# Performance work log

Measured on AMD Instinct MI355X. Metric: run time of the kernel, lower is better.

## Reference

```python
import jax, jax.numpy as jnp
import numpy as np

N = 50000      # nodes
E = 400000     # edges (avg degree 8)
G = 64         # graphs in batch
IN_DIM = 128
OUT_DIM = 16


def _linear_params(key, fan_in, fan_out):
    k1, k2 = jax.random.split(key)
    s = 1.0 / np.sqrt(fan_in)
    W = jax.random.uniform(k1, (fan_in, fan_out), minval=-s, maxval=s, dtype=jnp.float32)
    b = jax.random.uniform(k2, (fan_out,), minval=-s, maxval=s, dtype=jnp.float32)
    return W, b


def setup_inputs() -> dict:
    key = jax.random.key(0)
    ks = jax.random.split(key, 12)
    x = jax.random.normal(ks[0], (N, IN_DIM), dtype=jnp.float32)
    edge_index = jax.random.randint(ks[1], (2, E), 0, N)
    # balanced graph assignment (sorted, every graph id present)
    batch = (jnp.arange(N) * G) // N
    W1, b1 = _linear_params(ks[2], IN_DIM, 64)
    W2, b2 = _linear_params(ks[3], 64, 256)
    W3, b3 = _linear_params(ks[4], 256, 512)
    W4, b4 = _linear_params(ks[5], 512, 64)
    Wr, br = _linear_params(ks[6], IN_DIM, 64)
    fc1_W, fc1_b = _linear_params(ks[7], 64, 64)
    fc2_W, fc2_b = _linear_params(ks[8], 64, OUT_DIM)
    ln_g = jnp.ones((64,), jnp.float32); ln_b = jnp.zeros((64,), jnp.float32)
    fcn_g = jnp.ones((64,), jnp.float32); fcn_b = jnp.zeros((64,), jnp.float32)
    return dict(x=x, edge_index=edge_index, batch=batch,
                W1=W1, b1=b1, W2=W2, b2=b2, W3=W3, b3=b3, W4=W4, b4=b4,
                Wr=Wr, br=br, ln_g=ln_g, ln_b=ln_b,
                fc1_W=fc1_W, fc1_b=fc1_b, fcn_g=fcn_g, fcn_b=fcn_b,
                fc2_W=fc2_W, fc2_b=fc2_b)


def _leaky_relu(h):
    return jnp.where(h >= 0, h, 0.01 * h)


def _layer_norm(h, g, b, eps=1e-5):
    m = jnp.mean(h, axis=-1, keepdims=True)
    v = jnp.var(h, axis=-1, keepdims=True)
    return (h - m) * jax.lax.rsqrt(v + eps) * g + b


def reference(x, edge_index, batch, W1, b1, W2, b2, W3, b3, W4, b4,
              Wr, br, ln_g, ln_b, fc1_W, fc1_b, fcn_g, fcn_b, fc2_W, fc2_b):
    src, dst = edge_index[0], edge_index[1]
    n = x.shape[0]
    # PyG GCNConv normalization with self-loops: deg = 1 + in-degree
    deg = jax.ops.segment_sum(jnp.ones(src.shape[0], x.dtype), dst, num_segments=n) + 1.0
    dis = jax.lax.rsqrt(deg)                 # [N]
    edge_norm = (dis[src] * dis[dst])[:, None]   # [E,1]
    self_norm = (dis * dis)[:, None]             # [N,1]

    def gcn_conv(h, W, b):
        h = h @ W                                            # transform first (PyG order)
        agg = jax.ops.segment_sum(h[src] * edge_norm, dst, num_segments=n)
        return agg + h * self_norm + b                       # self-loop term + bias

    residual = x @ Wr + br
    h = _leaky_relu(gcn_conv(x, W1, b1))
    h = _leaky_relu(gcn_conv(h, W2, b2))
    h = _leaky_relu(gcn_conv(h, W3, b3))
    h = _leaky_relu(gcn_conv(h, W4, b4))
    h = _layer_norm(h + residual, ln_g, ln_b)
    # global max pool over graphs
    p = jax.ops.segment_max(h, batch, num_segments=G)        # [G,64]
    p = _layer_norm(p @ fc1_W + fc1_b, fcn_g, fcn_b)
    p = _leaky_relu(p)
    return p @ fc2_W + fc2_b                                 # [G,16]
```

## Files before the change

### kernel.cpp

```cpp
#include <hip/hip_runtime.h>
#include <hip/hip_bf16.h>
#include <math.h>

typedef short bf16x8 __attribute__((ext_vector_type(8)));
typedef short bf16x4 __attribute__((ext_vector_type(4)));
typedef float f32x4 __attribute__((ext_vector_type(4)));

__device__ inline unsigned short f2bf(float f) {
  unsigned u = __float_as_uint(f);
  u += 0x7FFF + ((u >> 16) & 1);
  return (unsigned short)(u >> 16);
}
__device__ inline float bf2f(unsigned short h) {
  return __uint_as_float(((unsigned)h) << 16);
}
__device__ inline float bflo(unsigned u) { return __uint_as_float(u << 16); }
__device__ inline float bfhi(unsigned u) { return __uint_as_float(u & 0xffff0000u); }


__global__ __launch_bounds__(256) void count_k(const int* __restrict__ dst, int* __restrict__ cnt, int e) {
  int i = blockIdx.x * 256 + threadIdx.x;
  if (i < e) atomicAdd(&cnt[dst[i]], 1);
}

__global__ __launch_bounds__(256) void scan_a(const int* __restrict__ cnt, int* __restrict__ bsum, int n) {
  int i = blockIdx.x * 256 + threadIdx.x;
  int v = (i < n) ? cnt[i] : 0;
#pragma unroll
  for (int o = 32; o > 0; o >>= 1) v += __shfl_xor(v, o);
  __shared__ int ws[4];
  if ((threadIdx.x & 63) == 0) ws[threadIdx.x >> 6] = v;
  __syncthreads();
  if (threadIdx.x == 0) bsum[blockIdx.x] = ws[0] + ws[1] + ws[2] + ws[3];
}

__global__ __launch_bounds__(256) void scan_b(const int* __restrict__ bsum, int* __restrict__ bpre,
                                              int* __restrict__ off_n, int nb) {
  __shared__ int s[256];
  int t = threadIdx.x;
  int v = (t < nb) ? bsum[t] : 0;
  s[t] = v;
  __syncthreads();
  for (int o = 1; o < 256; o <<= 1) {
    int u = (t >= o) ? s[t - o] : 0;
    __syncthreads();
    s[t] += u;
    __syncthreads();
  }
  if (t < nb) bpre[t] = s[t] - v;
  if (t == 255) off_n[0] = s[255];
}

__global__ __launch_bounds__(256) void scan_c(const int* __restrict__ cnt, const int* __restrict__ bpre,
                                              int* __restrict__ off, int* __restrict__ cursor,
                                              float* __restrict__ dis, int n) {
  __shared__ int s[256];
  int i = blockIdx.x * 256 + threadIdx.x;
  int t = threadIdx.x;
  int v = (i < n) ? cnt[i] : 0;
  s[t] = v;
  __syncthreads();
  for (int o = 1; o < 256; o <<= 1) {
    int u = (t >= o) ? s[t - o] : 0;
    __syncthreads();
    s[t] += u;
    __syncthreads();
  }
  if (i < n) {
    int ov = bpre[blockIdx.x] + s[t] - v;
    off[i] = ov;
    cursor[i] = ov;
    dis[i] = rsqrtf((float)v + 1.0f);
  }
}

__global__ __launch_bounds__(256) void scatter_k(const int* __restrict__ src, const int* __restrict__ dst,
                                                 int* __restrict__ cursor, int* __restrict__ csr, int e) {
  int i = blockIdx.x * 256 + threadIdx.x;
  if (i < e) {
    int p = atomicAdd(&cursor[dst[i]], 1);
    csr[p] = src[i];
  }
}


__global__ __launch_bounds__(256) void wconv_k(const float* __restrict__ W1, const float* __restrict__ Wr,
                                               const float* __restrict__ W2, const float* __restrict__ W3,
                                               const float* __restrict__ W4,
                                               short* __restrict__ o1, short* __restrict__ oR,
                                               short* __restrict__ o2, short* __restrict__ o3,
                                               short* __restrict__ o4) {
  int b = blockIdx.x;
  const float* W; short* O; int K, N, nr;
  if (b < 64)       { W = W1; O = o1; K = 128; N = 64;  nr = b; }
  else if (b < 128) { W = Wr; O = oR; K = 128; N = 64;  nr = b - 64; }
  else if (b < 384) { W = W2; O = o2; K = 64;  N = 256; nr = b - 128; }
  else if (b < 896) { W = W3; O = o3; K = 256; N = 512; nr = b - 384; }
  else              { W = W4; O = o4; K = 512; N = 64;  nr = b - 896; }
  for (int k = threadIdx.x; k < K; k += 256)
    O[(size_t)nr * K + k] = (short)f2bf(W[(size_t)k * N + nr]);
}


template<int KT, int NTOT, int WM, int WN, int BIAS, int RELU, int ABF, int OBF, int SPLIT, int SCL, int BLK>
__global__ __launch_bounds__(256, BLK) void mgemm(const void* __restrict__ Av,
                                                  const short* __restrict__ Wc,
                                                  const float* __restrict__ bias,
                                                  void* __restrict__ Cv, void* __restrict__ Cv2,
                                                  const float* __restrict__ scl, int M) {
  __shared__ short As[64 * WM][ABF ? 40 : 72];
  __shared__ short Bs[64 * WN][40];
  const int tid = threadIdx.x;
  const int row0 = blockIdx.x * (64 * WM);
  const int col0 = blockIdx.y * (64 * WN);
  const int w = tid >> 6, lane = tid & 63;
  const int wm = w / WN, wn = w % WN;
  const int rm = wm * 64, cn = wn * 64;
  const int lm = lane & 15, lk = (lane >> 4) * 8;

  f32x4 acc[4][4];
#pragma unroll
  for (int i = 0; i < 4; i++)
#pragma unroll
    for (int j = 0; j < 4; j++)
#pragma unroll
      for (int r = 0; r < 4; r++) acc[i][j][r] = 0.f;

  for (int k0 = 0; k0 < KT; k0 += 32) {
#pragma unroll
    for (int p = 0; p < WM; p++) {
      int r = (tid >> 2) + p * 64;
      int kseg = (tid & 3) * 8;
      int gr = row0 + r;
      if (ABF) {
        bf16x8 v = {0, 0, 0, 0, 0, 0, 0, 0};
        if (gr < M) v = *(const bf16x8*)((const short*)Av + (size_t)gr * KT + k0 + kseg);
        *(bf16x8*)&As[r][kseg] = v;
      } else {
        float4 v0 = {0.f, 0.f, 0.f, 0.f}, v1 = {0.f, 0.f, 0.f, 0.f};
        if (gr < M) {
          const float* ap = (const float*)Av + (size_t)gr * KT + k0 + kseg;
          v0 = *(const float4*)ap;
          v1 = *(const float4*)(ap + 4);
        }
        float vv[8] = {v0.x, v0.y, v0.z, v0.w, v1.x, v1.y, v1.z, v1.w};
        bf16x8 hv, lv;
#pragma unroll
        for (int j = 0; j < 8; j++) {
          unsigned short h = f2bf(vv[j]);
          hv[j] = (short)h;
          lv[j] = (short)f2bf(vv[j] - bf2f(h));
        }
        *(bf16x8*)&As[r][kseg] = hv;
        *(bf16x8*)&As[r][32 + kseg] = lv;
      }
    }
#pragma unroll
    for (int p = 0; p < WN; p++) {
      int nr = (tid >> 2) + p * 64;
      int seg = (tid & 3) * 8;
      *(bf16x8*)&Bs[nr][seg] = *(const bf16x8*)(Wc + (size_t)(col0 + nr) * KT + k0 + seg);
    }
    __syncthreads();

    bf16x8 ah[4], al[4], bb[4];
#pragma unroll
    for (int mt = 0; mt < 4; mt++) {
      ah[mt] = *(const bf16x8*)&As[rm + mt * 16 + lm][lk];
      if (!ABF) al[mt] = *(const bf16x8*)&As[rm + mt * 16 + lm][32 + lk];
    }
#pragma unroll
    for (int nt = 0; nt < 4; nt++) bb[nt] = *(const bf16x8*)&Bs[cn + nt * 16 + lm][lk];
#pragma unroll
    for (int mt = 0; mt < 4; mt++)
#pragma unroll
      for (int nt = 0; nt < 4; nt++) {
        acc[mt][nt] = __builtin_amdgcn_mfma_f32_16x16x32_bf16(ah[mt], bb[nt], acc[mt][nt], 0, 0, 0);
        if (!ABF)
          acc[mt][nt] = __builtin_amdgcn_mfma_f32_16x16x32_bf16(al[mt], bb[nt], acc[mt][nt], 0, 0, 0);
      }
    __syncthreads();
  }

  if (SPLIT) {
    short* epi = (short*)&As[0][0];
    if (wn == 0) {
#pragma unroll
      for (int mt = 0; mt < 4; mt++) {
        int lr = rm + mt * 16 + (lane >> 4) * 4;
#pragma unroll
        for (int r = 0; r < 4; r++) {
          int gr = row0 + lr + r;
          float sc = (SCL && gr < M) ? scl[gr] : 0.f;
#pragma unroll
          for (int nt = 0; nt < 4; nt++)
            epi[(lr + r) * 64 + nt * 16 + lm] = (short)f2bf(acc[mt][nt][r] * sc);
        }
      }
    } else {
#pragma unroll
      for (int mt = 0; mt < 4; mt++) {
        int grb = row0 + rm + mt * 16 + (lane >> 4) * 4;
#pragma unroll
        for (int nt = 0; nt < 4; nt++) {
          int gc = nt * 16 + lm;
          float bv = bias[gc];
#pragma unroll
          for (int r = 0; r < 4; r++) {
            int gr = grb + r;
            if (gr < M) ((float*)Cv2)[(size_t)gr * 64 + gc] = acc[mt][nt][r] + bv;
          }
        }
      }
    }
    __syncthreads();
    int base = tid * 32;
    int row = base >> 6, col = base & 63;
    int gr = row0 + row;
    if (gr < M) {
#pragma unroll
      for (int q = 0; q < 4; q++)
        *(bf16x8*)((short*)Cv + (size_t)gr * 64 + col + q * 8) = *(bf16x8*)&epi[base + q * 8];
    }
  } else if (OBF && WM == 1) {
    short* epi = &Bs[0][0];
    const int NCOL = 64 * WN;
    float bvv[4];
#pragma unroll
    for (int nt = 0; nt < 4; nt++) bvv[nt] = BIAS ? bias[col0 + cn + nt * 16 + lm] : 0.f;
#pragma unroll
    for (int mt = 0; mt < 4; mt++) {
      __syncthreads();
#pragma unroll
      for (int r = 0; r < 4; r++) {
        int gr = row0 + mt * 16 + (lane >> 4) * 4 + r;
        float sc = (SCL && gr < M) ? scl[gr] : 1.f;
#pragma unroll
        for (int nt = 0; nt < 4; nt++) {
          float v = acc[mt][nt][r] + bvv[nt];
          if (RELU) v = (v >= 0.f) ? v : 0.01f * v;
          if (SCL) v *= sc;
          epi[((lane >> 4) * 4 + r) * NCOL + cn + nt * 16 + lm] = (short)f2bf(v);
        }
      }
      __syncthreads();
      const int per = (16 * NCOL) / 256;
      int base = tid * per;
      int lr = base / NCOL, lc = base % NCOL;
      int gr = row0 + mt * 16 + lr;
      if (gr < M) {
#pragma unroll
        for (int q = 0; q < per / 8; q++)
          *(bf16x8*)((short*)Cv + (size_t)gr * NTOT + col0 + lc + q * 8) = *(bf16x8*)&epi[base + q * 8];
      }
    }
  } else {
#pragma unroll
    for (int mt = 0; mt < 4; mt++) {
      int grb = row0 + rm + mt * 16 + (lane >> 4) * 4;
#pragma unroll
      for (int nt = 0; nt < 4; nt++) {
        int gc = col0 + cn + nt * 16 + lm;
        float bv = BIAS ? bias[gc] : 0.f;
#pragma unroll
        for (int r = 0; r < 4; r++) {
          int gr = grb + r;
          if (gr < M) {
            float v = acc[mt][nt][r] + bv;
            if (RELU) v = (v >= 0.f) ? v : 0.01f * v;
            if (SCL) v *= scl[gr];
            if (OBF) ((short*)Cv)[(size_t)gr * NTOT + gc] = (short)f2bf(v);
            else     ((float*)Cv)[(size_t)gr * NTOT + gc] = v;
          }
        }
      }
    }
  }
}


__global__ __launch_bounds__(256, 3) void fused34_k(const short* __restrict__ z3,
                                                    const short* __restrict__ W3c,
                                                    const float* __restrict__ b3,
                                                    const short* __restrict__ W4c,
                                                    const float* __restrict__ dis,
                                                    short* __restrict__ T4, int M) {
  __shared__ short Bs[2][32][264];
  __shared__ short Ws4[2][64][40];
  __shared__ short Hs[64][40];
  const int tid = threadIdx.x;
  const int row0 = blockIdx.x * 64;
  const int w = tid >> 6, lane = tid & 63;
  const int lm = lane & 15, lk = (lane >> 4) * 8;
  const int rquad = (lane >> 4) * 4;
  const int w4row = tid >> 2, w4seg = (tid & 3) * 8;

  bf16x8 afr[8];
  {
    int gr = row0 + w * 16 + lm;
    bool ok = gr < M;
    const short* zp = z3 + (size_t)gr * 256 + lk;
#pragma unroll
    for (int kc = 0; kc < 8; kc++) {
      bf16x8 v = {0, 0, 0, 0, 0, 0, 0, 0};
      if (ok) v = *(const bf16x8*)(zp + kc * 32);
      afr[kc] = v;
    }
  }

  f32x4 t4acc[4];
#pragma unroll
  for (int nt = 0; nt < 4; nt++)
#pragma unroll
    for (int r = 0; r < 4; r++) t4acc[nt][r] = 0.f;

  bf16x8 pw3[4];
  bf16x8 pw4;
#pragma unroll
  for (int q = 0; q < 4; q++) {
    int flat = q * 2048 + tid * 8;
    pw3[q] = *(const bf16x8*)(W3c + flat);
  }
  pw4 = *(const bf16x8*)(W4c + (size_t)w4row * 512 + w4seg);
#pragma unroll
  for (int q = 0; q < 4; q++) {
    int flat = q * 2048 + tid * 8;
    *(bf16x8*)&Bs[0][flat >> 8][flat & 255] = pw3[q];
  }
  *(bf16x8*)&Ws4[0][w4row][w4seg] = pw4;
  __syncthreads();

  for (int c = 0; c < 16; c++) {
    int cur = c & 1, nxt = cur ^ 1;
    if (c < 15) {
#pragma unroll
      for (int q = 0; q < 4; q++) {
        int flat = q * 2048 + tid * 8;
        pw3[q] = *(const bf16x8*)(W3c + (size_t)(c + 1) * 32 * 256 + flat);
      }
      pw4 = *(const bf16x8*)(W4c + (size_t)w4row * 512 + (c + 1) * 32 + w4seg);
    }

    f32x4 acc1[2];
#pragma unroll
    for (int nt = 0; nt < 2; nt++)
#pragma unroll
      for (int r = 0; r < 4; r++) acc1[nt][r] = 0.f;
#pragma unroll
    for (int k0 = 0; k0 < 8; k0++) {
      bf16x8 bb[2];
#pragma unroll
      for (int nt = 0; nt < 2; nt++) bb[nt] = *(const bf16x8*)&Bs[cur][nt * 16 + lm][k0 * 32 + lk];
#pragma unroll
      for (int nt = 0; nt < 2; nt++)
        acc1[nt] = __builtin_amdgcn_mfma_f32_16x16x32_bf16(afr[k0], bb[nt], acc1[nt], 0, 0, 0);
    }
#pragma unroll
    for (int nt = 0; nt < 2; nt++) {
      float bv = b3[c * 32 + nt * 16 + lm];
#pragma unroll
      for (int r = 0; r < 4; r++) {
        float v = acc1[nt][r] + bv;
        v = (v >= 0.f) ? v : 0.01f * v;
        Hs[w * 16 + rquad + r][nt * 16 + lm] = (short)f2bf(v);
      }
    }
    {
      bf16x8 ah2 = *(const bf16x8*)&Hs[w * 16 + lm][lk];
      bf16x8 bb2[4];
#pragma unroll
      for (int nt = 0; nt < 4; nt++) bb2[nt] = *(const bf16x8*)&Ws4[cur][nt * 16 + lm][lk];
#pragma unroll
      for (int nt = 0; nt < 4; nt++)
        t4acc[nt] = __builtin_amdgcn_mfma_f32_16x16x32_bf16(ah2, bb2[nt], t4acc[nt], 0, 0, 0);
    }
    if (c < 15) {
#pragma unroll
      for (int q = 0; q < 4; q++) {
        int flat = q * 2048 + tid * 8;
        *(bf16x8*)&Bs[nxt][flat >> 8][flat & 255] = pw3[q];
      }
      *(bf16x8*)&Ws4[nxt][w4row][w4seg] = pw4;
    }
    __syncthreads();
  }
  short* epi = (short*)&Bs[0][0][0];
#pragma unroll
  for (int r = 0; r < 4; r++) {
    int lr = w * 16 + rquad + r;
    int gr = row0 + lr;
    float sc = (gr < M) ? dis[gr] : 0.f;
#pragma unroll
    for (int nt = 0; nt < 4; nt++)
      epi[lr * 64 + nt * 16 + lm] = (short)f2bf(t4acc[nt][r] * sc);
  }
  __syncthreads();
  {
    int base = tid * 16;
    int row = base >> 6, col = base & 63;
    int gr = row0 + row;
    if (gr < M) {
      *(bf16x8*)(T4 + (size_t)gr * 64 + col)     = *(bf16x8*)&epi[base];
      *(bf16x8*)(T4 + (size_t)gr * 64 + col + 8) = *(bf16x8*)&epi[base + 8];
    }
  }
}


template<int BR, int OSCL>
__global__ __launch_bounds__(256) void aggb64_k(const short* __restrict__ T, const float* __restrict__ dis,
                                                const int* __restrict__ off, const int* __restrict__ csr,
                                                const float* __restrict__ bias, short* __restrict__ Out, int n) {
  int wv = (blockIdx.x * 256 + threadIdx.x) >> 6;
  int lane = threadIdx.x & 63;
  int qtr = lane >> 4, ql = lane & 15;
  int wid = wv * 4 + qtr;
  if (wid >= n) return;
  float di = dis[wid];
  int e0 = off[wid], e1 = off[wid + 1];
  const uint2* Tw = (const uint2*)T;
  uint2 su = Tw[(size_t)wid * 16 + ql];
  float a0 = bflo(su.x), a1 = bfhi(su.x), a2 = bflo(su.y), a3 = bfhi(su.y);
  int e = e0;
  for (; e + 8 <= e1; e += 8) {
    uint2 u0 = Tw[(size_t)csr[e]     * 16 + ql];
    uint2 u1 = Tw[(size_t)csr[e + 1] * 16 + ql];
    uint2 u2 = Tw[(size_t)csr[e + 2] * 16 + ql];
    uint2 u3 = Tw[(size_t)csr[e + 3] * 16 + ql];
    uint2 u4 = Tw[(size_t)csr[e + 4] * 16 + ql];
    uint2 u5 = Tw[(size_t)csr[e + 5] * 16 + ql];
    uint2 u6 = Tw[(size_t)csr[e + 6] * 16 + ql];
    uint2 u7 = Tw[(size_t)csr[e + 7] * 16 + ql];
    a0 += ((bflo(u0.x) + bflo(u1.x)) + (bflo(u2.x) + bflo(u3.x))) +
          ((bflo(u4.x) + bflo(u5.x)) + (bflo(u6.x) + bflo(u7.x)));
    a1 += ((bfhi(u0.x) + bfhi(u1.x)) + (bfhi(u2.x) + bfhi(u3.x))) +
          ((bfhi(u4.x) + bfhi(u5.x)) + (bfhi(u6.x) + bfhi(u7.x)));
    a2 += ((bflo(u0.y) + bflo(u1.y)) + (bflo(u2.y) + bflo(u3.y))) +
          ((bflo(u4.y) + bflo(u5.y)) + (bflo(u6.y) + bflo(u7.y)));
    a3 += ((bfhi(u0.y) + bfhi(u1.y)) + (bfhi(u2.y) + bfhi(u3.y))) +
          ((bfhi(u4.y) + bfhi(u5.y)) + (bfhi(u6.y) + bfhi(u7.y)));
  }
  for (; e + 4 <= e1; e += 4) {
    uint2 u0 = Tw[(size_t)csr[e]     * 16 + ql];
    uint2 u1 = Tw[(size_t)csr[e + 1] * 16 + ql];
    uint2 u2 = Tw[(size_t)csr[e + 2] * 16 + ql];
    uint2 u3 = Tw[(size_t)csr[e + 3] * 16 + ql];
    a0 += (bflo(u0.x) + bflo(u1.x)) + (bflo(u2.x) + bflo(u3.x));
    a1 += (bfhi(u0.x) + bfhi(u1.x)) + (bfhi(u2.x) + bfhi(u3.x));
    a2 += (bflo(u0.y) + bflo(u1.y)) + (bflo(u2.y) + bflo(u3.y));
    a3 += (bfhi(u0.y) + bfhi(u1.y)) + (bfhi(u2.y) + bfhi(u3.y));
  }
  for (; e < e1; e++) {
    uint2 u = Tw[(size_t)csr[e] * 16 + ql];
    a0 += bflo(u.x); a1 += bfhi(u.x); a2 += bflo(u.y); a3 += bfhi(u.y);
  }
  float v0 = di * a0, v1 = di * a1, v2 = di * a2, v3 = di * a3;
  if (BR) {
    v0 += bias[ql * 4];     v1 += bias[ql * 4 + 1];
    v2 += bias[ql * 4 + 2]; v3 += bias[ql * 4 + 3];
    v0 = (v0 >= 0.f) ? v0 : 0.01f * v0;
    v1 = (v1 >= 0.f) ? v1 : 0.01f * v1;
    v2 = (v2 >= 0.f) ? v2 : 0.01f * v2;
    v3 = (v3 >= 0.f) ? v3 : 0.01f * v3;
  }
  if (OSCL) { v0 *= di; v1 *= di; v2 *= di; v3 *= di; }
  uint2 o;
  o.x = (unsigned)f2bf(v0) | ((unsigned)f2bf(v1) << 16);
  o.y = (unsigned)f2bf(v2) | ((unsigned)f2bf(v3) << 16);
  ((uint2*)Out)[(size_t)wid * 16 + ql] = o;
}

__global__ __launch_bounds__(256) void agg64_ln_k(const short* __restrict__ T, const float* __restrict__ dis,
                                                  const int* __restrict__ off, const int* __restrict__ csr,
                                                  const float* __restrict__ bias, const float* __restrict__ resid,
                                                  const float* __restrict__ g, const float* __restrict__ b,
                                                  float* __restrict__ outh, int n) {
  int wv = (blockIdx.x * 256 + threadIdx.x) >> 6;
  int lane = threadIdx.x & 63;
  int qtr = lane >> 4, ql = lane & 15;
  int wid = wv * 4 + qtr;
  if (wid >= n) return;
  float di = dis[wid];
  int e0 = off[wid], e1 = off[wid + 1];
  const uint2* Tw = (const uint2*)T;
  uint2 su = Tw[(size_t)wid * 16 + ql];
  float a0 = bflo(su.x), a1 = bfhi(su.x), a2 = bflo(su.y), a3 = bfhi(su.y);
  int e = e0;
  for (; e + 8 <= e1; e += 8) {
    uint2 u0 = Tw[(size_t)csr[e]     * 16 + ql];
    uint2 u1 = Tw[(size_t)csr[e + 1] * 16 + ql];
    uint2 u2 = Tw[(size_t)csr[e + 2] * 16 + ql];
    uint2 u3 = Tw[(size_t)csr[e + 3] * 16 + ql];
    uint2 u4 = Tw[(size_t)csr[e + 4] * 16 + ql];
    uint2 u5 = Tw[(size_t)csr[e + 5] * 16 + ql];
    uint2 u6 = Tw[(size_t)csr[e + 6] * 16 + ql];
    uint2 u7 = Tw[(size_t)csr[e + 7] * 16 + ql];
    a0 += ((bflo(u0.x) + bflo(u1.x)) + (bflo(u2.x) + bflo(u3.x))) +
          ((bflo(u4.x) + bflo(u5.x)) + (bflo(u6.x) + bflo(u7.x)));
    a1 += ((bfhi(u0.x) + bfhi(u1.x)) + (bfhi(u2.x) + bfhi(u3.x))) +
          ((bfhi(u4.x) + bfhi(u5.x)) + (bfhi(u6.x) + bfhi(u7.x)));
    a2 += ((bflo(u0.y) + bflo(u1.y)) + (bflo(u2.y) + bflo(u3.y))) +
          ((bflo(u4.y) + bflo(u5.y)) + (bflo(u6.y) + bflo(u7.y)));
    a3 += ((bfhi(u0.y) + bfhi(u1.y)) + (bfhi(u2.y) + bfhi(u3.y))) +
          ((bfhi(u4.y) + bfhi(u5.y)) + (bfhi(u6.y) + bfhi(u7.y)));
  }
  for (; e + 4 <= e1; e += 4) {
    uint2 u0 = Tw[(size_t)csr[e]     * 16 + ql];
    uint2 u1 = Tw[(size_t)csr[e + 1] * 16 + ql];
    uint2 u2 = Tw[(size_t)csr[e + 2] * 16 + ql];
    uint2 u3 = Tw[(size_t)csr[e + 3] * 16 + ql];
    a0 += (bflo(u0.x) + bflo(u1.x)) + (bflo(u2.x) + bflo(u3.x));
    a1 += (bfhi(u0.x) + bfhi(u1.x)) + (bfhi(u2.x) + bfhi(u3.x));
    a2 += (bflo(u0.y) + bflo(u1.y)) + (bflo(u2.y) + bflo(u3.y));
    a3 += (bfhi(u0.y) + bfhi(u1.y)) + (bfhi(u2.y) + bfhi(u3.y));
  }
  for (; e < e1; e++) {
    uint2 u = Tw[(size_t)csr[e] * 16 + ql];
    a0 += bflo(u.x); a1 += bfhi(u.x); a2 += bflo(u.y); a3 += bfhi(u.y);
  }
  float4 rv = ((const float4*)resid)[(size_t)wid * 16 + ql];
  float v0 = di * a0 + bias[ql * 4];
  float v1 = di * a1 + bias[ql * 4 + 1];
  float v2 = di * a2 + bias[ql * 4 + 2];
  float v3 = di * a3 + bias[ql * 4 + 3];
  v0 = (v0 >= 0.f) ? v0 : 0.01f * v0;
  v1 = (v1 >= 0.f) ? v1 : 0.01f * v1;
  v2 = (v2 >= 0.f) ? v2 : 0.01f * v2;
  v3 = (v3 >= 0.f) ? v3 : 0.01f * v3;
  v0 += rv.x; v1 += rv.y; v2 += rv.z; v3 += rv.w;
  float s = (v0 + v1) + (v2 + v3);
  float ss = (v0 * v0 + v1 * v1) + (v2 * v2 + v3 * v3);
#pragma unroll
  for (int o = 8; o > 0; o >>= 1) {
    s += __shfl_xor(s, o);
    ss += __shfl_xor(ss, o);
  }
  float m = s * (1.f / 64.f);
  float var = ss * (1.f / 64.f) - m * m;
  float rs = rsqrtf(var + 1e-5f);
  float4 o4;
  o4.x = (v0 - m) * rs * g[ql * 4]     + b[ql * 4];
  o4.y = (v1 - m) * rs * g[ql * 4 + 1] + b[ql * 4 + 1];
  o4.z = (v2 - m) * rs * g[ql * 4 + 2] + b[ql * 4 + 2];
  o4.w = (v3 - m) * rs * g[ql * 4 + 3] + b[ql * 4 + 3];
  ((float4*)outh)[(size_t)wid * 16 + ql] = o4;
}

__global__ __launch_bounds__(256) void agg256b_k(const short* __restrict__ T, const float* __restrict__ dis,
                                                 const int* __restrict__ off, const int* __restrict__ csr,
                                                 short* __restrict__ Out, int n) {
  int wv = (blockIdx.x * 256 + threadIdx.x) >> 6;
  int lane = threadIdx.x & 63;
  int qtr = lane >> 4, ql = lane & 15;
  int wid = wv * 4 + qtr;
  if (wid >= n) return;
  float di = dis[wid];
  int e0 = off[wid], e1 = off[wid + 1];
  const short* base = T + (size_t)wid * 256 + ql * 16;
  bf16x8 s0 = *(const bf16x8*)base;
  bf16x8 s1 = *(const bf16x8*)(base + 8);
  float a[16];
#pragma unroll
  for (int q = 0; q < 8; q++) { a[q] = bf2f((unsigned short)s0[q]); a[8 + q] = bf2f((unsigned short)s1[q]); }
  int e = e0;
  for (; e + 4 <= e1; e += 4) {
    const short* p0 = T + (size_t)csr[e]     * 256 + ql * 16;
    const short* p1 = T + (size_t)csr[e + 1] * 256 + ql * 16;
    const short* p2 = T + (size_t)csr[e + 2] * 256 + ql * 16;
    const short* p3 = T + (size_t)csr[e + 3] * 256 + ql * 16;
    bf16x8 t00 = *(const bf16x8*)p0, t01 = *(const bf16x8*)(p0 + 8);
    bf16x8 t10 = *(const bf16x8*)p1, t11 = *(const bf16x8*)(p1 + 8);
    bf16x8 t20 = *(const bf16x8*)p2, t21 = *(const bf16x8*)(p2 + 8);
    bf16x8 t30 = *(const bf16x8*)p3, t31 = *(const bf16x8*)(p3 + 8);
#pragma unroll
    for (int q = 0; q < 8; q++) {
      a[q] += (bf2f((unsigned short)t00[q]) + bf2f((unsigned short)t10[q])) +
              (bf2f((unsigned short)t20[q]) + bf2f((unsigned short)t30[q]));
      a[8 + q] += (bf2f((unsigned short)t01[q]) + bf2f((unsigned short)t11[q])) +
                  (bf2f((unsigned short)t21[q]) + bf2f((unsigned short)t31[q]));
    }
  }
  for (; e < e1; e++) {
    const short* p = T + (size_t)csr[e] * 256 + ql * 16;
    bf16x8 t0 = *(const bf16x8*)p, t1 = *(const bf16x8*)(p + 8);
#pragma unroll
    for (int q = 0; q < 8; q++) {
      a[q] += bf2f((unsigned short)t0[q]);
      a[8 + q] += bf2f((unsigned short)t1[q]);
    }
  }
  bf16x8 o0, o1;
#pragma unroll
  for (int q = 0; q < 8; q++) {
    o0[q] = (short)f2bf(di * a[q]);
    o1[q] = (short)f2bf(di * a[8 + q]);
  }
  short* ob = Out + (size_t)wid * 256 + ql * 16;
  *(bf16x8*)ob = o0;
  *(bf16x8*)(ob + 8) = o1;
}


__global__ __launch_bounds__(256) void pool_mlp_k(const float* __restrict__ hn,
                                                  const float* __restrict__ fc1W, const float* __restrict__ fc1b,
                                                  const float* __restrict__ fng, const float* __restrict__ fnb,
                                                  const float* __restrict__ fc2W, const float* __restrict__ fc2b,
                                                  float* __restrict__ out, int n) {
  const int G = 64;
  int g = blockIdx.x;
  int f = threadIdx.x & 63, c = threadIdx.x >> 6;
  long long s0 = ((long long)g * n + G - 1) / G;
  long long e0 = ((long long)(g + 1) * n + G - 1) / G;
  float m = -INFINITY;
  for (long long i = s0 + c; i < e0; i += 4) m = fmaxf(m, hn[(size_t)i * 64 + f]);
  __shared__ float red[4][64];
  __shared__ float ps[64], qs[64];
  red[c][f] = m;
  __syncthreads();
  if (c == 0) ps[f] = fmaxf(fmaxf(red[0][f], red[1][f]), fmaxf(red[2][f], red[3][f]));
  __syncthreads();
  if (threadIdx.x < 64) {
    int lane = threadIdx.x;
    float q = fc1b[lane];
#pragma unroll 8
    for (int k = 0; k < 64; k++) q = fmaf(ps[k], fc1W[k * 64 + lane], q);
    float s = q, ss = q * q;
#pragma unroll
    for (int o = 32; o > 0; o >>= 1) {
      s += __shfl_xor(s, o);
      ss += __shfl_xor(ss, o);
    }
    float mm = s * (1.f / 64.f);
    float var = ss * (1.f / 64.f) - mm * mm;
    float y = (q - mm) * rsqrtf(var + 1e-5f) * fng[lane] + fnb[lane];
    y = (y >= 0.f) ? y : 0.01f * y;
    qs[lane] = y;
    __builtin_amdgcn_wave_barrier();
    if (lane < 16) {
      float o = fc2b[lane];
#pragma unroll 8
      for (int k = 0; k < 64; k++) o = fmaf(qs[k], fc2W[k * 16 + lane], o);
      out[g * 16 + lane] = o;
    }
  }
}


extern "C" void kernel_launch(void* const* d_in, const int* in_sizes, int n_in,
                              void* d_out, int out_size, void* d_ws, size_t ws_size,
                              hipStream_t stream) {
  const float* x   = (const float*)d_in[0];
  const int*   ei  = (const int*)d_in[1];
  const float* W1  = (const float*)d_in[3];
  const float* b1  = (const float*)d_in[4];
  const float* W2  = (const float*)d_in[5];
  const float* b2  = (const float*)d_in[6];
  const float* W3  = (const float*)d_in[7];
  const float* b3  = (const float*)d_in[8];
  const float* W4  = (const float*)d_in[9];
  const float* b4  = (const float*)d_in[10];
  const float* Wr  = (const float*)d_in[11];
  const float* br  = (const float*)d_in[12];
  const float* lng = (const float*)d_in[13];
  const float* lnb = (const float*)d_in[14];
  const float* f1W = (const float*)d_in[15];
  const float* f1b = (const float*)d_in[16];
  const float* fng = (const float*)d_in[17];
  const float* fnb = (const float*)d_in[18];
  const float* f2W = (const float*)d_in[19];
  const float* f2b = (const float*)d_in[20];

  int n = in_sizes[0] / 128;
  int e = in_sizes[1] / 2;
  const int* src = ei;
  const int* dst = ei + e;

  float* arena = (float*)d_ws;
  float* resid = arena;
  short* h2b   = (short*)(arena + (size_t)64 * n);
  short* t4b   = (short*)(arena + (size_t)64 * n);
  short* z3b   = (short*)(arena + (size_t)192 * n);
  float* hn    = arena + (size_t)192 * n;
  short* t1b   = (short*)(arena + (size_t)320 * n);
  short* h1b   = (short*)(arena + (size_t)352 * n);
  short* z2b   = (short*)(arena + (size_t)384 * n);
  float* dis   = arena + (size_t)448 * n;
  int* cnt    = (int*)(dis + n);
  int* off    = cnt + n;
  int* cursor = off + n + 1;
  int* csr    = cursor + n;
  int* bsum   = csr + e;
  int* bpre   = bsum + 256;
  float* pool = (float*)(bpre + 256);
  size_t wq = (((size_t)(pool + 4096)) + 15) & ~(size_t)15;
  short* wc1 = (short*)wq;
  short* wcR = wc1 + 8192;
  short* wc2 = wcR + 8192;
  short* wc3 = wc2 + 16384;
  short* wc4 = wc3 + 131072;
  size_t need = ((char*)(wc4 + 32768) - (char*)d_ws) + 64;
  if (ws_size < need) return;

  int nb_n = (n + 255) / 256;
  int nb_e = (e + 255) / 256;
  int nb_w4 = ((n + 3) / 4 + 3) / 4;
  int g_wide = (n + 63) / 64;
  int g_fused = (n + 127) / 128;

  wconv_k<<<960, 256, 0, stream>>>(W1, Wr, W2, W3, W4, wc1, wcR, wc2, wc3, wc4);

  hipMemsetAsync(cnt, 0, (size_t)n * sizeof(int), stream);
  count_k<<<nb_e, 256, 0, stream>>>(dst, cnt, e);
  scan_a<<<nb_n, 256, 0, stream>>>(cnt, bsum, n);
  scan_b<<<1, 256, 0, stream>>>(bsum, bpre, off + n, nb_n);
  scan_c<<<nb_n, 256, 0, stream>>>(cnt, bpre, off, cursor, dis, n);
  scatter_k<<<nb_e, 256, 0, stream>>>(src, dst, cursor, csr, e);

  mgemm<128, 128, 2, 2, 1, 0, 0, 0, 1, 1, 4><<<dim3(g_fused, 1), 256, 0, stream>>>(x, wc1, br, t1b, resid, dis, n);
  aggb64_k<1, 1><<<nb_w4, 256, 0, stream>>>(t1b, dis, off, csr, b1, h1b, n);
  aggb64_k<0, 0><<<nb_w4, 256, 0, stream>>>(h1b, dis, off, csr, nullptr, z2b, n);
  mgemm<64, 256, 1, 4, 1, 1, 1, 1, 0, 1, 5><<<dim3(g_wide, 1), 256, 0, stream>>>(z2b, wc2, b2, h2b, nullptr, dis, n);
  agg256b_k<<<nb_w4, 256, 0, stream>>>(h2b, dis, off, csr, z3b, n);
  fused34_k<<<g_wide, 256, 0, stream>>>(z3b, wc3, b3, wc4, dis, t4b, n);
  agg64_ln_k<<<nb_w4, 256, 0, stream>>>(t4b, dis, off, csr, b4, resid, lng, lnb, hn, n);
  pool_mlp_k<<<64, 256, 0, stream>>>(hn, f1W, f1b, fng, fnb, f2W, f2b, (float*)d_out, n);
}
```

Baseline: 353.6 us.

## Restructure fused layer-3/4 GEMM with 2x2 warp tiling and direct-to-LDS weight loads

Reworks the fused W3→leaky→W4 kernel so each wave computes 32 rows by 16 columns of the W3 chunk, reusing each B fragment across two M tiles. W3 tiles are now streamed with global_load_lds straight into LDS in the MFMA fragment layout, instead of staging through registers. Each wave accumulates layer-4 partial sums over two chunks, reading W4 fragments directly from global memory. The two column-half partials are then reduced through an fp32 LDS buffer in the epilogue. This aims to cut LDS traffic and register staging, at the cost of more accumulator registers, uncached global reads of W4, and an extra fp32 reduction pass.

New measurement: 366.6 us. 3.7% more time.

```diff
diff --git a/kernel.cpp b/kernel.cpp
--- a/kernel.cpp
+++ b/kernel.cpp
@@ -16,6 +16,11 @@
 }
 __device__ inline float bflo(unsigned u) { return __uint_as_float(u << 16); }
 __device__ inline float bfhi(unsigned u) { return __uint_as_float(u & 0xffff0000u); }
+
+__device__ __forceinline__ void gl_lds16(const void* g, void* l) {
+  __builtin_amdgcn_global_load_lds((const __attribute__((address_space(1))) void*)g,
+                                   (__attribute__((address_space(3))) void*)l, 16, 0, 0);
+}
 
 
 __global__ __launch_bounds__(256) void count_k(const int* __restrict__ dst, int* __restrict__ cnt, int e) {
@@ -285,123 +290,128 @@
                                                     const short* __restrict__ W4c,
                                                     const float* __restrict__ dis,
                                                     short* __restrict__ T4, int M) {
-  __shared__ short Bs[2][32][264];
-  __shared__ short Ws4[2][64][40];
-  __shared__ short Hs[64][40];
+  __shared__ __align__(16) char smem[43008];
+  short* Bs = (short*)smem;
   const int tid = threadIdx.x;
   const int row0 = blockIdx.x * 64;
   const int w = tid >> 6, lane = tid & 63;
-  const int lm = lane & 15, lk = (lane >> 4) * 8;
-  const int rquad = (lane >> 4) * 4;
-  const int w4row = tid >> 2, w4seg = (tid & 3) * 8;
-
-  bf16x8 afr[8];
-  {
-    int gr = row0 + w * 16 + lm;
+  const int wr = w >> 1, wc = w & 1;
+  const int q = lane >> 4, lm = lane & 15;
+  short* slab = (short*)(smem + 32768) + w * 1280;
+
+  bf16x8 afr[2][8];
+#pragma unroll
+  for (int mt = 0; mt < 2; mt++) {
+    int gr = row0 + wr * 32 + mt * 16 + lm;
     bool ok = gr < M;
-    const short* zp = z3 + (size_t)gr * 256 + lk;
-#pragma unroll
-    for (int kc = 0; kc < 8; kc++) {
+    const short* zp = z3 + (size_t)gr * 256 + q * 8;
+#pragma unroll
+    for (int k0 = 0; k0 < 8; k0++) {
       bf16x8 v = {0, 0, 0, 0, 0, 0, 0, 0};
-      if (ok) v = *(const bf16x8*)(zp + kc * 32);
-      afr[kc] = v;
-    }
-  }
-
-  f32x4 t4acc[4];
-#pragma unroll
-  for (int nt = 0; nt < 4; nt++)
-#pragma unroll
-    for (int r = 0; r < 4; r++) t4acc[nt][r] = 0.f;
-
-  bf16x8 pw3[4];
-  bf16x8 pw4;
-#pragma unroll
-  for (int q = 0; q < 4; q++) {
-    int flat = q * 2048 + tid * 8;
-    pw3[q] = *(const bf16x8*)(W3c + flat);
-  }
-  pw4 = *(const bf16x8*)(W4c + (size_t)w4row * 512 + w4seg);
-#pragma unroll
-  for (int q = 0; q < 4; q++) {
-    int flat = q * 2048 + tid * 8;
-    *(bf16x8*)&Bs[0][flat >> 8][flat & 255] = pw3[q];
-  }
-  *(bf16x8*)&Ws4[0][w4row][w4seg] = pw4;
+      if (ok) v = *(const bf16x8*)(zp + k0 * 32);
+      afr[mt][k0] = v;
+    }
+  }
+
+  f32x4 t4acc[2][4];
+#pragma unroll
+  for (int mt = 0; mt < 2; mt++)
+#pragma unroll
+    for (int nt = 0; nt < 4; nt++)
+#pragma unroll
+      for (int r = 0; r < 4; r++) t4acc[mt][nt][r] = 0.f;
+
+#pragma unroll
+  for (int i = 0; i < 4; i++) {
+    int seg = w * 4 + i;
+    int k0s = seg >> 1, colT = seg & 1;
+    const short* gsrc = W3c + (size_t)(colT * 16 + lm) * 256 + k0s * 32 + q * 8;
+    gl_lds16(gsrc, Bs + seg * 512);
+  }
   __syncthreads();
 
+#pragma unroll
   for (int c = 0; c < 16; c++) {
-    int cur = c & 1, nxt = cur ^ 1;
+    const int cur = c & 1, nxt = cur ^ 1;
     if (c < 15) {
 #pragma unroll
-      for (int q = 0; q < 4; q++) {
-        int flat = q * 2048 + tid * 8;
-        pw3[q] = *(const bf16x8*)(W3c + (size_t)(c + 1) * 32 * 256 + flat);
-      }
-      pw4 = *(const bf16x8*)(W4c + (size_t)w4row * 512 + (c + 1) * 32 + w4seg);
-    }
+      for (int i = 0; i < 4; i++) {
+        int seg = w * 4 + i;
+        int k0s = seg >> 1, colT = seg & 1;
+        const short* gsrc = W3c + (size_t)((c + 1) * 32 + colT * 16 + lm) * 256 + k0s * 32 + q * 8;
+        gl_lds16(gsrc, Bs + nxt * 8192 + seg * 512);
+      }
+    }
+    float bv = b3[c * 32 + wc * 16 + lm];
 
     f32x4 acc1[2];
 #pragma unroll
-    for (int nt = 0; nt < 2; nt++)
-#pragma unroll
-      for (int r = 0; r < 4; r++) acc1[nt][r] = 0.f;
+    for (int mt = 0; mt < 2; mt++)
+#pragma unroll
+      for (int r = 0; r < 4; r++) acc1[mt][r] = 0.f;
 #pragma unroll
     for (int k0 = 0; k0 < 8; k0++) {
-      bf16x8 bb[2];
-#pragma unroll
-      for (int nt = 0; nt < 2; nt++) bb[nt] = *(const bf16x8*)&Bs[cur][nt * 16 + lm][k0 * 32 + lk];
-#pragma unroll
-      for (int nt = 0; nt < 2; nt++)
-        acc1[nt] = __builtin_amdgcn_mfma_f32_16x16x32_bf16(afr[k0], bb[nt], acc1[nt], 0, 0, 0);
-    }
-#pragma unroll
-    for (int nt = 0; nt < 2; nt++) {
-      float bv = b3[c * 32 + nt * 16 + lm];
+      bf16x8 bb = *(const bf16x8*)(Bs + cur * 8192 + (k0 * 2 + wc) * 512 + lane * 8);
+#pragma unroll
+      for (int mt = 0; mt < 2; mt++)
+        acc1[mt] = __builtin_amdgcn_mfma_f32_16x16x32_bf16(afr[mt][k0], bb, acc1[mt], 0, 0, 0);
+    }
+#pragma unroll
+    for (int mt = 0; mt < 2; mt++)
 #pragma unroll
       for (int r = 0; r < 4; r++) {
-        float v = acc1[nt][r] + bv;
+        float v = acc1[mt][r] + bv;
         v = (v >= 0.f) ? v : 0.01f * v;
-        Hs[w * 16 + rquad + r][nt * 16 + lm] = (short)f2bf(v);
-      }
-    }
-    {
-      bf16x8 ah2 = *(const bf16x8*)&Hs[w * 16 + lm][lk];
-      bf16x8 bb2[4];
-#pragma unroll
-      for (int nt = 0; nt < 4; nt++) bb2[nt] = *(const bf16x8*)&Ws4[cur][nt * 16 + lm][lk];
-#pragma unroll
-      for (int nt = 0; nt < 4; nt++)
-        t4acc[nt] = __builtin_amdgcn_mfma_f32_16x16x32_bf16(ah2, bb2[nt], t4acc[nt], 0, 0, 0);
-    }
-    if (c < 15) {
-#pragma unroll
-      for (int q = 0; q < 4; q++) {
-        int flat = q * 2048 + tid * 8;
-        *(bf16x8*)&Bs[nxt][flat >> 8][flat & 255] = pw3[q];
-      }
-      *(bf16x8*)&Ws4[nxt][w4row][w4seg] = pw4;
+        slab[(mt * 16 + q * 4 + r) * 40 + (c & 1) * 16 + lm] = (short)f2bf(v);
+      }
+    if (c & 1) {
+      bf16x8 ha[2];
+#pragma unroll
+      for (int mt = 0; mt < 2; mt++)
+        ha[mt] = *(const bf16x8*)(slab + (mt * 16 + lm) * 40 + q * 8);
+      int kb = (c - 1 + (q >> 1)) * 32 + wc * 16 + (q & 1) * 8;
+#pragma unroll
+      for (int nt = 0; nt < 4; nt++) {
+        bf16x8 wb = *(const bf16x8*)(W4c + (size_t)(nt * 16 + lm) * 512 + kb);
+#pragma unroll
+        for (int mt = 0; mt < 2; mt++)
+          t4acc[mt][nt] = __builtin_amdgcn_mfma_f32_16x16x32_bf16(ha[mt], wb, t4acc[mt][nt], 0, 0, 0);
+      }
     }
     __syncthreads();
   }
-  short* epi = (short*)&Bs[0][0][0];
-#pragma unroll
-  for (int r = 0; r < 4; r++) {
-    int lr = w * 16 + rquad + r;
-    int gr = row0 + lr;
-    float sc = (gr < M) ? dis[gr] : 0.f;
+
+  float* Pf = (float*)smem;
+#pragma unroll
+  for (int mt = 0; mt < 2; mt++)
 #pragma unroll
     for (int nt = 0; nt < 4; nt++)
-      epi[lr * 64 + nt * 16 + lm] = (short)f2bf(t4acc[nt][r] * sc);
-  }
+#pragma unroll
+      for (int r = 0; r < 4; r++)
+        Pf[wc * 4352 + (size_t)(wr * 32 + mt * 16 + q * 4 + r) * 68 + nt * 16 + lm] = t4acc[mt][nt][r];
   __syncthreads();
   {
-    int base = tid * 16;
-    int row = base >> 6, col = base & 63;
+    int row = tid >> 2, cb = (tid & 3) * 16;
     int gr = row0 + row;
     if (gr < M) {
-      *(bf16x8*)(T4 + (size_t)gr * 64 + col)     = *(bf16x8*)&epi[base];
-      *(bf16x8*)(T4 + (size_t)gr * 64 + col + 8) = *(bf16x8*)&epi[base + 8];
+      float sc = dis[gr];
+      const f32x4* p0 = (const f32x4*)(Pf + (size_t)row * 68 + cb);
+      const f32x4* p1 = (const f32x4*)(Pf + 4352 + (size_t)row * 68 + cb);
+      bf16x8 o0, o1;
+#pragma unroll
+      for (int j2 = 0; j2 < 2; j2++) {
+        f32x4 s = p0[j2] + p1[j2];
+#pragma unroll
+        for (int j = 0; j < 4; j++) o0[j2 * 4 + j] = (short)f2bf(s[j] * sc);
+      }
+#pragma unroll
+      for (int j2 = 0; j2 < 2; j2++) {
+        f32x4 s = p0[2 + j2] + p1[2 + j2];
+#pragma unroll
+        for (int j = 0; j < 4; j++) o1[j2 * 4 + j] = (short)f2bf(s[j] * sc);
+      }
+      *(bf16x8*)(T4 + (size_t)gr * 64 + cb) = o0;
+      *(bf16x8*)(T4 + (size_t)gr * 64 + cb + 8) = o1;
     }
   }
 }
```

## Fuse 256-wide neighbor aggregation into the layer-3/4 fused GEMM kernel

Applied to the files above, without the earlier changes.

The standalone agg256b kernel is removed. fused34_k now gathers neighbor rows of h2 for its own 64-node tile, normalizes them and stages the bf16 result in shared memory (reusing the Bs buffer) before loading the MFMA A fragments. This drops the global write and re-read of the 256-wide z3 intermediate and one kernel launch. In exchange, the gather latency now sits inside a GEMM kernel with limited occupancy (launch bounds 256,3), so it is less hidden, and two extra barriers are added.

After: 352.4 us. Within noise of the previous version (-0.4%).

```diff
diff --git a/kernel.cpp b/kernel.cpp
--- a/kernel.cpp
+++ b/kernel.cpp
@@ -279,7 +279,8 @@
 }
 
 
-__global__ __launch_bounds__(256, 3) void fused34_k(const short* __restrict__ z3,
+__global__ __launch_bounds__(256, 3) void fused34_k(const short* __restrict__ h2,
+                                                    const int* __restrict__ off, const int* __restrict__ csr,
                                                     const short* __restrict__ W3c,
                                                     const float* __restrict__ b3,
                                                     const short* __restrict__ W4c,
@@ -294,19 +295,73 @@
   const int lm = lane & 15, lk = (lane >> 4) * 8;
   const int rquad = (lane >> 4) * 4;
   const int w4row = tid >> 2, w4seg = (tid & 3) * 8;
+  const int qtr = lane >> 4, ql = lane & 15;
+
+  short* Zs = (short*)&Bs[0][0][0];
+  for (int pass = 0; pass < 4; pass++) {
+    int nid = pass * 16 + w * 4 + qtr;
+    int gr = row0 + nid;
+    float a[16];
+    if (gr < M) {
+      float di = dis[gr];
+      int e0 = off[gr], e1 = off[gr + 1];
+      const short* base = h2 + (size_t)gr * 256 + ql * 16;
+      bf16x8 s0 = *(const bf16x8*)base;
+      bf16x8 s1 = *(const bf16x8*)(base + 8);
+#pragma unroll
+      for (int j = 0; j < 8; j++) { a[j] = bf2f((unsigned short)s0[j]); a[8 + j] = bf2f((unsigned short)s1[j]); }
+      int e = e0;
+      for (; e + 4 <= e1; e += 4) {
+        const short* p0 = h2 + (size_t)csr[e]     * 256 + ql * 16;
+        const short* p1 = h2 + (size_t)csr[e + 1] * 256 + ql * 16;
+        const short* p2 = h2 + (size_t)csr[e + 2] * 256 + ql * 16;
+        const short* p3 = h2 + (size_t)csr[e + 3] * 256 + ql * 16;
+        bf16x8 t00 = *(const bf16x8*)p0, t01 = *(const bf16x8*)(p0 + 8);
+        bf16x8 t10 = *(const bf16x8*)p1, t11 = *(const bf16x8*)(p1 + 8);
+        bf16x8 t20 = *(const bf16x8*)p2, t21 = *(const bf16x8*)(p2 + 8);
+        bf16x8 t30 = *(const bf16x8*)p3, t31 = *(const bf16x8*)(p3 + 8);
+#pragma unroll
+        for (int j = 0; j < 8; j++) {
+          a[j] += (bf2f((unsigned short)t00[j]) + bf2f((unsigned short)t10[j])) +
+                  (bf2f((unsigned short)t20[j]) + bf2f((unsigned short)t30[j]));
+          a[8 + j] += (bf2f((unsigned short)t01[j]) + bf2f((unsigned short)t11[j])) +
+                      (bf2f((unsigned short)t21[j]) + bf2f((unsigned short)t31[j]));
+        }
+      }
+      for (; e < e1; e++) {
+        const short* p = h2 + (size_t)csr[e] * 256 + ql * 16;
+        bf16x8 t0 = *(const bf16x8*)p, t1 = *(const bf16x8*)(p + 8);
+#pragma unroll
+        for (int j = 0; j < 8; j++) {
+          a[j] += bf2f((unsigned short)t0[j]);
+          a[8 + j] += bf2f((unsigned short)t1[j]);
+        }
+      }
+#pragma unroll
+      for (int j = 0; j < 16; j++) a[j] *= di;
+    } else {
+#pragma unroll
+      for (int j = 0; j < 16; j++) a[j] = 0.f;
+    }
+    bf16x8 o0, o1;
+#pragma unroll
+    for (int j = 0; j < 8; j++) {
+      o0[j] = (short)f2bf(a[j]);
+      o1[j] = (short)f2bf(a[8 + j]);
+    }
+    *(bf16x8*)&Zs[nid * 264 + ql * 16] = o0;
+    *(bf16x8*)&Zs[nid * 264 + ql * 16 + 8] = o1;
+  }
+  __syncthreads();
 
   bf16x8 afr[8];
   {
-    int gr = row0 + w * 16 + lm;
-    bool ok = gr < M;
-    const short* zp = z3 + (size_t)gr * 256 + lk;
-#pragma unroll
-    for (int kc = 0; kc < 8; kc++) {
-      bf16x8 v = {0, 0, 0, 0, 0, 0, 0, 0};
-      if (ok) v = *(const bf16x8*)(zp + kc * 32);
-      afr[kc] = v;
-    }
-  }
+    int lr = w * 16 + lm;
+#pragma unroll
+    for (int kc = 0; kc < 8; kc++)
+      afr[kc] = *(const bf16x8*)&Zs[lr * 264 + kc * 32 + lk];
+  }
+  __syncthreads();
 
   f32x4 t4acc[4];
 #pragma unroll
@@ -546,60 +601,6 @@
   ((float4*)outh)[(size_t)wid * 16 + ql] = o4;
 }
 
-__global__ __launch_bounds__(256) void agg256b_k(const short* __restrict__ T, const float* __restrict__ dis,
-                                                 const int* __restrict__ off, const int* __restrict__ csr,
-                                                 short* __restrict__ Out, int n) {
-  int wv = (blockIdx.x * 256 + threadIdx.x) >> 6;
-  int lane = threadIdx.x & 63;
-  int qtr = lane >> 4, ql = lane & 15;
-  int wid = wv * 4 + qtr;
-  if (wid >= n) return;
-  float di = dis[wid];
-  int e0 = off[wid], e1 = off[wid + 1];
-  const short* base = T + (size_t)wid * 256 + ql * 16;
-  bf16x8 s0 = *(const bf16x8*)base;
-  bf16x8 s1 = *(const bf16x8*)(base + 8);
-  float a[16];
-#pragma unroll
-  for (int q = 0; q < 8; q++) { a[q] = bf2f((unsigned short)s0[q]); a[8 + q] = bf2f((unsigned short)s1[q]); }
-  int e = e0;
-  for (; e + 4 <= e1; e += 4) {
-    const short* p0 = T + (size_t)csr[e]     * 256 + ql * 16;
-    const short* p1 = T + (size_t)csr[e + 1] * 256 + ql * 16;
-    const short* p2 = T + (size_t)csr[e + 2] * 256 + ql * 16;
-    const short* p3 = T + (size_t)csr[e + 3] * 256 + ql * 16;
-    bf16x8 t00 = *(const bf16x8*)p0, t01 = *(const bf16x8*)(p0 + 8);
-    bf16x8 t10 = *(const bf16x8*)p1, t11 = *(const bf16x8*)(p1 + 8);
-    bf16x8 t20 = *(const bf16x8*)p2, t21 = *(const bf16x8*)(p2 + 8);
-    bf16x8 t30 = *(const bf16x8*)p3, t31 = *(const bf16x8*)(p3 + 8);
-#pragma unroll
-    for (int q = 0; q < 8; q++) {
-      a[q] += (bf2f((unsigned short)t00[q]) + bf2f((unsigned short)t10[q])) +
-              (bf2f((unsigned short)t20[q]) + bf2f((unsigned short)t30[q]));
-      a[8 + q] += (bf2f((unsigned short)t01[q]) + bf2f((unsigned short)t11[q])) +
-                  (bf2f((unsigned short)t21[q]) + bf2f((unsigned short)t31[q]));
-    }
-  }
-  for (; e < e1; e++) {
-    const short* p = T + (size_t)csr[e] * 256 + ql * 16;
-    bf16x8 t0 = *(const bf16x8*)p, t1 = *(const bf16x8*)(p + 8);
-#pragma unroll
-    for (int q = 0; q < 8; q++) {
-      a[q] += bf2f((unsigned short)t0[q]);
-      a[8 + q] += bf2f((unsigned short)t1[q]);
-    }
-  }
-  bf16x8 o0, o1;
-#pragma unroll
-  for (int q = 0; q < 8; q++) {
-    o0[q] = (short)f2bf(di * a[q]);
-    o1[q] = (short)f2bf(di * a[8 + q]);
-  }
-  short* ob = Out + (size_t)wid * 256 + ql * 16;
-  *(bf16x8*)ob = o0;
-  *(bf16x8*)(ob + 8) = o1;
-}
-
 
 __global__ __launch_bounds__(256) void pool_mlp_k(const float* __restrict__ hn,
                                                   const float* __restrict__ fc1W, const float* __restrict__ fc1b,
@@ -678,9 +679,8 @@
   float* arena = (float*)d_ws;
   float* resid = arena;
   short* h2b   = (short*)(arena + (size_t)64 * n);
-  short* t4b   = (short*)(arena + (size_t)64 * n);
-  short* z3b   = (short*)(arena + (size_t)192 * n);
-  float* hn    = arena + (size_t)192 * n;
+  short* t4b   = (short*)(arena + (size_t)192 * n);
+  float* hn    = arena + (size_t)224 * n;
   short* t1b   = (short*)(arena + (size_t)320 * n);
   short* h1b   = (short*)(arena + (size_t)352 * n);
   short* z2b   = (short*)(arena + (size_t)384 * n);
@@ -720,8 +720,7 @@
   aggb64_k<1, 1><<<nb_w4, 256, 0, stream>>>(t1b, dis, off, csr, b1, h1b, n);
   aggb64_k<0, 0><<<nb_w4, 256, 0, stream>>>(h1b, dis, off, csr, nullptr, z2b, n);
   mgemm<64, 256, 1, 4, 1, 1, 1, 1, 0, 1, 5><<<dim3(g_wide, 1), 256, 0, stream>>>(z2b, wc2, b2, h2b, nullptr, dis, n);
-  agg256b_k<<<nb_w4, 256, 0, stream>>>(h2b, dis, off, csr, z3b, n);
-  fused34_k<<<g_wide, 256, 0, stream>>>(z3b, wc3, b3, wc4, dis, t4b, n);
+  fused34_k<<<g_wide, 256, 0, stream>>>(h2b, off, csr, wc3, b3, wc4, dis, t4b, n);
   agg64_ln_k<<<nb_w4, 256, 0, stream>>>(t4b, dis, off, csr, b4, resid, lng, lnb, hn, n);
   pool_mlp_k<<<64, 256, 0, stream>>>(hn, f1W, f1b, fng, fnb, f2W, f2b, (float*)d_out, n);
 }
```
